# Performance work log

Hardware: AMD Instinct MI355X
Metric: run time of the kernel (lower is better)

## Reference

```python
import jax, jax.numpy as jnp
import numpy as np

N0, N1, N2 = 20000, 15000, 15000
N = N0 + N1 + N2          # total nodes
E = 800000                # edges
H, D = 4, 64              # heads, hidden per head
ED = 64                   # edge feature dim
NET = 8                   # num edge types
C = 16                    # num classes
SLOPE = 0.2               # leaky relu negative slope
ALPHA = 0.05              # residual-attention mixing

def _glorot(key, shape):
    return jax.random.normal(key, shape, dtype=jnp.float32) / jnp.sqrt(jnp.float32(shape[-1]))

def setup_inputs() -> dict:
    key = jax.random.key(0)
    ks = jax.random.split(key, 32)
    return {
        "x0": jax.random.normal(ks[0], (N0, 128), jnp.float32),
        "x1": jax.random.normal(ks[1], (N1, 64), jnp.float32),
        "x2": jax.random.normal(ks[2], (N2, 32), jnp.float32),
        "src": jax.random.randint(ks[3], (E,), 0, N),
        "dst": jax.random.randint(ks[4], (E,), 0, N),
        "efeat": jax.random.randint(ks[5], (E,), 0, NET),
        # per-node-type input projections (fc_list)
        "W0": _glorot(ks[6], (64, 128)), "b0": jnp.zeros((64,), jnp.float32),
        "W1": _glorot(ks[7], (64, 64)),  "b1": jnp.zeros((64,), jnp.float32),
        "W2": _glorot(ks[8], (64, 32)),  "b2": jnp.zeros((64,), jnp.float32),
        # GAT layer 0: in 64 -> H*D, no residual, elu
        "Wg0": _glorot(ks[9], (H * D, 64)),
        "etab0": _glorot(ks[10], (NET, ED)),
        "We0": _glorot(ks[11], (H * ED, ED)),
        "al0": _glorot(ks[12], (H, D)), "ar0": _glorot(ks[13], (H, D)), "ae0": _glorot(ks[14], (H, ED)),
        # GAT layer 1: in H*D -> H*D, identity residual, elu
        "Wg1": _glorot(ks[15], (H * D, H * D)),
        "etab1": _glorot(ks[16], (NET, ED)),
        "We1": _glorot(ks[17], (H * ED, ED)),
        "al1": _glorot(ks[18], (H, D)), "ar1": _glorot(ks[19], (H, D)), "ae1": _glorot(ks[20], (H, ED)),
        # final GAT layer: in H*D -> 1*C, linear residual, no activation
        "Wg2": _glorot(ks[21], (C, H * D)),
        "etab2": _glorot(ks[22], (NET, ED)),
        "We2": _glorot(ks[23], (ED, ED)),
        "al2": _glorot(ks[24], (1, C)), "ar2": _glorot(ks[25], (1, C)), "ae2": _glorot(ks[26], (1, ED)),
        "resW2": _glorot(ks[27], (C, H * D)),
    }

def _edge_softmax(scores, dst):
    # softmax over incoming edges of each dst node; scores: [E, H]
    m = jax.ops.segment_max(scores, dst, num_segments=N)
    ex = jnp.exp(scores - m[dst])
    s = jax.ops.segment_sum(ex, dst, num_segments=N)
    return ex / (s[dst] + 1e-9)

def _gat_conv(h, src, dst, et, Wg, etab, We, al, ar, ae, res_attn, res, resW, act):
    nH, oD = al.shape
    feat = (h @ Wg.T).reshape(N, nH, oD)                 # [N,H,D]
    ee = (etab[et] @ We.T).reshape(E, nH, -1)            # [E,H,ED]
    el = jnp.einsum('nhd,hd->nh', feat, al)
    er = jnp.einsum('nhd,hd->nh', feat, ar)
    es = jnp.einsum('ehd,hd->eh', ee, ae)
    logits = jax.nn.leaky_relu(el[src] + er[dst] + es, SLOPE)
    a = _edge_softmax(logits, dst)                       # [E,H]
    if res_attn is not None:
        a = a * (1.0 - ALPHA) + res_attn * ALPHA
    out = jax.ops.segment_sum(a[:, :, None] * feat[src], dst, num_segments=N)
    if res:
        resval = (h @ resW.T).reshape(N, -1, oD) if resW is not None else h.reshape(N, nH, oD)
        out = out + resval
    if act is not None:
        out = act(out)
    return out, jax.lax.stop_gradient(a)                 # attention detached (res_attn)

def reference(x0, x1, x2, src, dst, efeat, W0, b0, W1, b1, W2, b2,
              Wg0, etab0, We0, al0, ar0, ae0,
              Wg1, etab1, We1, al1, ar1, ae1,
              Wg2, etab2, We2, al2, ar2, ae2, resW2):
    h = jnp.concatenate([x0 @ W0.T + b0, x1 @ W1.T + b1, x2 @ W2.T + b2], axis=0)  # [N,64]
    h, ra = _gat_conv(h, src, dst, efeat, Wg0, etab0, We0, al0, ar0, ae0, None, False, None, jax.nn.elu)
    h = h.reshape(N, -1)
    h, ra = _gat_conv(h, src, dst, efeat, Wg1, etab1, We1, al1, ar1, ae1, ra, True, None, jax.nn.elu)
    h = h.reshape(N, -1)
    logits, _ = _gat_conv(h, src, dst, efeat, Wg2, etab2, We2, al2, ar2, ae2, None, True, resW2, None)
    return logits.mean(axis=1)                           # [N, C]
```

## Files before the change

### kernel.cpp

```cpp
#include <hip/hip_runtime.h>
#include <math.h>

#define N0 20000
#define N1 15000
#define N2 15000
#define NN 50000
#define EE 800000
#define SLOPE 0.2f
#define ALPHA 0.05f

typedef _Float16 h8 __attribute__((ext_vector_type(8)));
typedef _Float16 h4 __attribute__((ext_vector_type(4)));
typedef float f4v __attribute__((ext_vector_type(4)));

__device__ __forceinline__ float sel4(float4 v, int h) {
    float lo = (h & 1) ? v.y : v.x;
    float hi = (h & 1) ? v.w : v.z;
    return (h & 2) ? hi : lo;
}

__device__ __forceinline__ float elu_fast(float x) {
    return x > 0.f ? x : __expf(x) - 1.f;
}


__global__ void hist_kernel(const int* __restrict__ dst, int* __restrict__ deg, int E_) {
    int e = blockIdx.x * blockDim.x + threadIdx.x;
    if (e < E_) atomicAdd(&deg[dst[e]], 1);
}

__global__ __launch_bounds__(256) void block_sum_kernel(const int* __restrict__ deg,
                                                        int* __restrict__ bsum, int n) {
    int i = blockIdx.x * 256 + threadIdx.x;
    int v = (i < n) ? deg[i] : 0;
    #pragma unroll
    for (int off = 32; off > 0; off >>= 1) v += __shfl_down(v, off);
    __shared__ int sh[4];
    if ((threadIdx.x & 63) == 0) sh[threadIdx.x >> 6] = v;
    __syncthreads();
    if (threadIdx.x == 0) bsum[blockIdx.x] = sh[0] + sh[1] + sh[2] + sh[3];
}

__global__ __launch_bounds__(256) void scan_bsum_kernel(int* __restrict__ bsum, int nb) {
    __shared__ int sh[256];
    int tid = threadIdx.x;
    int v = (tid < nb) ? bsum[tid] : 0;
    sh[tid] = v;
    __syncthreads();
    #pragma unroll
    for (int off = 1; off < 256; off <<= 1) {
        int t = (tid >= off) ? sh[tid - off] : 0;
        __syncthreads();
        sh[tid] += t;
        __syncthreads();
    }
    if (tid < nb) bsum[tid] = sh[tid] - v;
}

__global__ __launch_bounds__(256) void scan_out_kernel(const int* __restrict__ deg,
                                                       const int* __restrict__ boff,
                                                       int* __restrict__ rowstart,
                                                       int* __restrict__ cursor, int n) {
    __shared__ int sh[256];
    int tid = threadIdx.x;
    int i = blockIdx.x * 256 + tid;
    int v = (i < n) ? deg[i] : 0;
    sh[tid] = v;
    __syncthreads();
    #pragma unroll
    for (int off = 1; off < 256; off <<= 1) {
        int t = (tid >= off) ? sh[tid - off] : 0;
        __syncthreads();
        sh[tid] += t;
        __syncthreads();
    }
    int excl = sh[tid] - v + boff[blockIdx.x];
    if (i < n) { rowstart[i] = excl; cursor[i] = excl; }
    if (i == n - 1) rowstart[n] = excl + v;
}

__global__ void scatter_kernel(const int* __restrict__ src, const int* __restrict__ dst,
                               const int* __restrict__ et, int* __restrict__ cursor,
                               int* __restrict__ pk, int E_) {
    int e = blockIdx.x * blockDim.x + threadIdx.x;
    if (e >= E_) return;
    int d = dst[e];
    int p = atomicAdd(&cursor[d], 1);
    pk[p] = (et[e] << 16) | src[e];
}


__global__ void es_table_all(const float* __restrict__ etab0, const float* __restrict__ We0,
                             const float* __restrict__ ae0,
                             const float* __restrict__ etab1, const float* __restrict__ We1,
                             const float* __restrict__ ae1,
                             const float* __restrict__ etab2, const float* __restrict__ We2,
                             const float* __restrict__ ae2,
                             float* __restrict__ es) {
    int b = blockIdx.x;
    const float *etab, *We, *ae;
    float* out;
    int H;
    if (b < 32)      { etab = etab0; We = We0; ae = ae0; out = es;      H = 4; }
    else if (b < 64) { b -= 32; etab = etab1; We = We1; ae = ae1; out = es + 32; H = 4; }
    else             { b -= 64; etab = etab2; We = We2; ae = ae2; out = es + 64; H = 1; }
    int t = b / H, h = b % H;
    int j = threadIdx.x;
    const float* w = We + (size_t)(h * 64 + j) * 64;
    const float* e = etab + t * 64;
    float s = 0.f;
    #pragma unroll
    for (int k = 0; k < 64; k += 4) {
        float4 wv = *(const float4*)(w + k);
        float4 ev = *(const float4*)(e + k);
        s += wv.x * ev.x + wv.y * ev.y + wv.z * ev.z + wv.w * ev.w;
    }
    s *= ae[h * 64 + j];
    #pragma unroll
    for (int off = 32; off > 0; off >>= 1) s += __shfl_down(s, off);
    if (j == 0) out[t * H + h] = s;
}


__global__ void f2h10(const float* s0, _Float16* d0, int n0,
                      const float* s1, _Float16* d1, int n1,
                      const float* s2, _Float16* d2, int n2,
                      const float* s3, _Float16* d3, int n3,
                      const float* s4, _Float16* d4, int n4,
                      const float* s5, _Float16* d5, int n5,
                      const float* s6, _Float16* d6, int n6,
                      const float* s7, _Float16* d7, int n7,
                      const float* s8, _Float16* d8, int n8,
                      const float* s9, _Float16* d9, int n9) {
    int t = blockIdx.x * 256 + threadIdx.x;
    if (t < n0) { d0[t] = (_Float16)s0[t]; return; } t -= n0;
    if (t < n1) { d1[t] = (_Float16)s1[t]; return; } t -= n1;
    if (t < n2) { d2[t] = (_Float16)s2[t]; return; } t -= n2;
    if (t < n3) { d3[t] = (_Float16)s3[t]; return; } t -= n3;
    if (t < n4) { d4[t] = (_Float16)s4[t]; return; } t -= n4;
    if (t < n5) { d5[t] = (_Float16)s5[t]; return; } t -= n5;
    if (t < n6) { d6[t] = (_Float16)s6[t]; return; } t -= n6;
    if (t < n7) { d7[t] = (_Float16)s7[t]; return; } t -= n7;
    if (t < n8) { d8[t] = (_Float16)s8[t]; return; } t -= n8;
    if (t < n9) { d9[t] = (_Float16)s9[t]; }
}


template<int NT>
__global__ __launch_bounds__(256) void gemm_mfma(const _Float16* __restrict__ A,
                                                 const _Float16* __restrict__ B,
                                                 const float* __restrict__ bias,
                                                 float* __restrict__ Cf,
                                                 _Float16* __restrict__ Ch,
                                                 int M, int N, int K) {
    const int wave = threadIdx.x >> 6;
    const int lane = threadIdx.x & 63;
    const int m_base = (blockIdx.x * 4 + wave) * 32;
    const int n_base = blockIdx.y * (NT * 16);
    const int row = lane & 15;
    const int kq = (lane >> 4) * 8;

    f4v acc[2][NT];
    #pragma unroll
    for (int i = 0; i < 2; i++)
        #pragma unroll
        for (int j = 0; j < NT; j++) {
            f4v z = {0.f, 0.f, 0.f, 0.f};
            acc[i][j] = z;
        }

    int r0 = m_base + row;      if (r0 >= M) r0 = M - 1;
    int r1 = m_base + 16 + row; if (r1 >= M) r1 = M - 1;
    const _Float16* a0p = A + (size_t)r0 * K + kq;
    const _Float16* a1p = A + (size_t)r1 * K + kq;
    const _Float16* bp  = B + (size_t)(n_base + row) * K + kq;

    for (int k = 0; k < K; k += 32) {
        h8 a0 = *(const h8*)(a0p + k);
        h8 a1 = *(const h8*)(a1p + k);
        #pragma unroll
        for (int j = 0; j < NT; j++) {
            h8 b = *(const h8*)(bp + (size_t)j * 16 * K + k);
            acc[0][j] = __builtin_amdgcn_mfma_f32_16x16x32_f16(a0, b, acc[0][j], 0, 0, 0);
            acc[1][j] = __builtin_amdgcn_mfma_f32_16x16x32_f16(a1, b, acc[1][j], 0, 0, 0);
        }
    }

    const int col = lane & 15;
    const int rb = (lane >> 4) * 4;
    #pragma unroll
    for (int ms = 0; ms < 2; ms++) {
        #pragma unroll
        for (int j = 0; j < NT; j++) {
            #pragma unroll
            for (int r = 0; r < 4; r++) {
                int m = m_base + ms * 16 + rb + r;
                if (m < M) {
                    int n = n_base + j * 16 + col;
                    float v = acc[ms][j][r];
                    if (bias) v += bias[n];
                    if (Cf) Cf[(size_t)m * N + n] = v;
                    if (Ch) Ch[(size_t)m * N + n] = (_Float16)v;
                }
            }
        }
    }
}


__global__ void node_elr_h(const _Float16* __restrict__ feat, const float* __restrict__ al,
                           const float* __restrict__ ar, float* __restrict__ el,
                           float* __restrict__ er, int nN) {
    int t = blockIdx.x * blockDim.x + threadIdx.x;
    if (t >= nN * 4) return;
    int n = t >> 2, h = t & 3;
    const _Float16* f = feat + (size_t)n * 256 + h * 64;
    const float* a = al + h * 64;
    const float* r = ar + h * 64;
    float sl = 0.f, sr = 0.f;
    #pragma unroll
    for (int j = 0; j < 64; j += 8) {
        h8 fv = *(const h8*)(f + j);
        #pragma unroll
        for (int q = 0; q < 8; q++) {
            float x = (float)fv[q];
            sl = fmaf(x, a[j + q], sl);
            sr = fmaf(x, r[j + q], sr);
        }
    }
    el[t] = sl; er[t] = sr;
}

__global__ void node_elr_f2(const float* __restrict__ feat, const float* __restrict__ al,
                            const float* __restrict__ ar, float* __restrict__ el,
                            float* __restrict__ er, int nN) {
    int t = blockIdx.x * blockDim.x + threadIdx.x;
    if (t >= nN) return;
    const float* f = feat + (size_t)t * 32;
    float sl = 0.f, sr = 0.f;
    #pragma unroll
    for (int j = 0; j < 16; j += 4) {
        float4 fv = *(const float4*)(f + j);
        float4 av = *(const float4*)(al + j);
        float4 rv = *(const float4*)(ar + j);
        sl += fv.x * av.x + fv.y * av.y + fv.z * av.z + fv.w * av.w;
        sr += fv.x * rv.x + fv.y * rv.y + fv.z * rv.z + fv.w * rv.w;
    }
    el[t] = sl; er[t] = sr;
}


template<bool WRITE_A, bool HAS_PREV, bool HAS_RES>
__global__ __launch_bounds__(256) void gat_fused4(const int* __restrict__ rowstart,
                                                  const int* __restrict__ pk,
                                                  const float* __restrict__ el,
                                                  const float* __restrict__ er,
                                                  const float* __restrict__ es,
                                                  const _Float16* __restrict__ feat,
                                                  const _Float16* __restrict__ aprev,
                                                  _Float16* __restrict__ awrite,
                                                  const _Float16* __restrict__ resh,
                                                  _Float16* __restrict__ outh, int nN) {
    __shared__ int2 as_lds[4][256];
    const int wave = threadIdx.x >> 6;
    const int lane = threadIdx.x & 63;
    int n = blockIdx.x * 4 + wave;
    if (n >= nN) return;
    const int r0 = rowstart[n], r1 = rowstart[n + 1];
    const int deg = r1 - r0;
    float4 er4 = *(const float4*)(er + n * 4);

    if (deg <= 64) {
        const int idx = r0 + lane;
        const bool act = idx < r1;
        int p = act ? pk[idx] : 0;
        int psrc = p & 0xFFFF;
        float4 v4 = {-INFINITY, -INFINITY, -INFINITY, -INFINITY};
        if (act) {
            float4 e4 = *(const float4*)(el + psrc * 4);
            float4 c4 = *(const float4*)(es + (p >> 16) * 4);
            float v;
            v = e4.x + er4.x + c4.x; v4.x = v > 0.f ? v : SLOPE * v;
            v = e4.y + er4.y + c4.y; v4.y = v > 0.f ? v : SLOPE * v;
            v = e4.z + er4.z + c4.z; v4.z = v > 0.f ? v : SLOPE * v;
            v = e4.w + er4.w + c4.w; v4.w = v > 0.f ? v : SLOPE * v;
        }
        float4 m4 = v4;
        #pragma unroll
        for (int off = 1; off <= 8; off <<= 1) {
            m4.x = fmaxf(m4.x, __shfl_xor(m4.x, off));
            m4.y = fmaxf(m4.y, __shfl_xor(m4.y, off));
            m4.z = fmaxf(m4.z, __shfl_xor(m4.z, off));
            m4.w = fmaxf(m4.w, __shfl_xor(m4.w, off));
        }
        if (deg > 16) {
            m4.x = fmaxf(m4.x, __shfl_xor(m4.x, 16));
            m4.y = fmaxf(m4.y, __shfl_xor(m4.y, 16));
            m4.z = fmaxf(m4.z, __shfl_xor(m4.z, 16));
            m4.w = fmaxf(m4.w, __shfl_xor(m4.w, 16));
        }
        if (deg > 32) {
            m4.x = fmaxf(m4.x, __shfl_xor(m4.x, 32));
            m4.y = fmaxf(m4.y, __shfl_xor(m4.y, 32));
            m4.z = fmaxf(m4.z, __shfl_xor(m4.z, 32));
            m4.w = fmaxf(m4.w, __shfl_xor(m4.w, 32));
        }
        float4 ex = {0.f, 0.f, 0.f, 0.f};
        if (act) {
            ex.x = __expf(v4.x - m4.x);
            ex.y = __expf(v4.y - m4.y);
            ex.z = __expf(v4.z - m4.z);
            ex.w = __expf(v4.w - m4.w);
        }
        float4 s4 = ex;
        #pragma unroll
        for (int off = 1; off <= 8; off <<= 1) {
            s4.x += __shfl_xor(s4.x, off);
            s4.y += __shfl_xor(s4.y, off);
            s4.z += __shfl_xor(s4.z, off);
            s4.w += __shfl_xor(s4.w, off);
        }
        if (deg > 16) {
            s4.x += __shfl_xor(s4.x, 16);
            s4.y += __shfl_xor(s4.y, 16);
            s4.z += __shfl_xor(s4.z, 16);
            s4.w += __shfl_xor(s4.w, 16);
        }
        if (deg > 32) {
            s4.x += __shfl_xor(s4.x, 32);
            s4.y += __shfl_xor(s4.y, 32);
            s4.z += __shfl_xor(s4.z, 32);
            s4.w += __shfl_xor(s4.w, 32);
        }
        float4 a4;
        a4.x = ex.x / (s4.x + 1e-9f);
        a4.y = ex.y / (s4.y + 1e-9f);
        a4.z = ex.z / (s4.z + 1e-9f);
        a4.w = ex.w / (s4.w + 1e-9f);
        if (HAS_PREV && act) {
            h4 pv = *(const h4*)(aprev + (size_t)idx * 4);
            a4.x = a4.x * (1.f - ALPHA) + ALPHA * (float)pv[0];
            a4.y = a4.y * (1.f - ALPHA) + ALPHA * (float)pv[1];
            a4.z = a4.z * (1.f - ALPHA) + ALPHA * (float)pv[2];
            a4.w = a4.w * (1.f - ALPHA) + ALPHA * (float)pv[3];
        }
        if (WRITE_A && act) {
            h4 aw;
            aw[0] = (_Float16)a4.x; aw[1] = (_Float16)a4.y;
            aw[2] = (_Float16)a4.z; aw[3] = (_Float16)a4.w;
            *(h4*)(awrite + (size_t)idx * 4) = aw;
        }
        {
            int2* dst_lds = &as_lds[wave][lane * 4];
            dst_lds[0] = make_int2(__float_as_int(a4.x), psrc);
            dst_lds[1] = make_int2(__float_as_int(a4.y), psrc);
            dst_lds[2] = make_int2(__float_as_int(a4.z), psrc);
            dst_lds[3] = make_int2(__float_as_int(a4.w), psrc);
        }

        const int half = lane >> 5;
        const int fl = lane & 31;
        const int h = fl >> 3;
        float acc8[8];
        #pragma unroll
        for (int q = 0; q < 8; q++) acc8[q] = 0.f;
        int i = r0;
        for (; i + 7 < r1; i += 8) {
            int j0 = (i - r0) + half;
            int2 e0 = as_lds[wave][(j0 + 0) * 4 + h];
            int2 e1 = as_lds[wave][(j0 + 2) * 4 + h];
            int2 e2 = as_lds[wave][(j0 + 4) * 4 + h];
            int2 e3 = as_lds[wave][(j0 + 6) * 4 + h];
            float a0 = __int_as_float(e0.x), a1 = __int_as_float(e1.x);
            float a2 = __int_as_float(e2.x), a3 = __int_as_float(e3.x);
            h8 f0 = *(const h8*)(feat + (size_t)e0.y * 256 + fl * 8);
            h8 f1 = *(const h8*)(feat + (size_t)e1.y * 256 + fl * 8);
            h8 f2 = *(const h8*)(feat + (size_t)e2.y * 256 + fl * 8);
            h8 f3 = *(const h8*)(feat + (size_t)e3.y * 256 + fl * 8);
            #pragma unroll
            for (int q = 0; q < 8; q++) acc8[q] = fmaf(a0, (float)f0[q], acc8[q]);
            #pragma unroll
            for (int q = 0; q < 8; q++) acc8[q] = fmaf(a1, (float)f1[q], acc8[q]);
            #pragma unroll
            for (int q = 0; q < 8; q++) acc8[q] = fmaf(a2, (float)f2[q], acc8[q]);
            #pragma unroll
            for (int q = 0; q < 8; q++) acc8[q] = fmaf(a3, (float)f3[q], acc8[q]);
        }
        for (; i + 3 < r1; i += 4) {
            int j0 = (i - r0) + half;
            int2 e0 = as_lds[wave][(j0 + 0) * 4 + h];
            int2 e1 = as_lds[wave][(j0 + 2) * 4 + h];
            float a0 = __int_as_float(e0.x), a1 = __int_as_float(e1.x);
            h8 f0 = *(const h8*)(feat + (size_t)e0.y * 256 + fl * 8);
            h8 f1 = *(const h8*)(feat + (size_t)e1.y * 256 + fl * 8);
            #pragma unroll
            for (int q = 0; q < 8; q++) acc8[q] = fmaf(a0, (float)f0[q], acc8[q]);
            #pragma unroll
            for (int q = 0; q < 8; q++) acc8[q] = fmaf(a1, (float)f1[q], acc8[q]);
        }
        for (; i + 1 < r1; i += 2) {
            int j0 = (i - r0) + half;
            int2 e0 = as_lds[wave][j0 * 4 + h];
            float a0 = __int_as_float(e0.x);
            h8 f0 = *(const h8*)(feat + (size_t)e0.y * 256 + fl * 8);
            #pragma unroll
            for (int q = 0; q < 8; q++) acc8[q] = fmaf(a0, (float)f0[q], acc8[q]);
        }
        if (i < r1) {
            int j0 = i - r0;
            int2 e0 = as_lds[wave][j0 * 4 + h];
            float a0 = (half == 0) ? __int_as_float(e0.x) : 0.f;
            h8 f0 = *(const h8*)(feat + (size_t)e0.y * 256 + fl * 8);
            #pragma unroll
            for (int q = 0; q < 8; q++) acc8[q] = fmaf(a0, (float)f0[q], acc8[q]);
        }
        #pragma unroll
        for (int q = 0; q < 8; q++) acc8[q] += __shfl_xor(acc8[q], 32);

        if (half == 0) {
            if (HAS_RES) {
                h8 rv = *(const h8*)(resh + (size_t)n * 256 + fl * 8);
                #pragma unroll
                for (int q = 0; q < 8; q++) acc8[q] += (float)rv[q];
            }
            #pragma unroll
            for (int q = 0; q < 8; q++) acc8[q] = elu_fast(acc8[q]);
            h8 o;
            #pragma unroll
            for (int q = 0; q < 8; q++) o[q] = (_Float16)acc8[q];
            *(h8*)(outh + (size_t)n * 256 + fl * 8) = o;
        }
        return;
    }

    float4 m4 = {-INFINITY, -INFINITY, -INFINITY, -INFINITY};
    for (int base = r0; base < r1; base += 64) {
        int idx = base + lane;
        if (idx < r1) {
            int p = pk[idx];
            float4 e4 = *(const float4*)(el + (p & 0xFFFF) * 4);
            float4 c4 = *(const float4*)(es + (p >> 16) * 4);
            float v;
            v = e4.x + er4.x + c4.x; v = v > 0.f ? v : SLOPE * v; m4.x = fmaxf(m4.x, v);
            v = e4.y + er4.y + c4.y; v = v > 0.f ? v : SLOPE * v; m4.y = fmaxf(m4.y, v);
            v = e4.z + er4.z + c4.z; v = v > 0.f ? v : SLOPE * v; m4.z = fmaxf(m4.z, v);
            v = e4.w + er4.w + c4.w; v = v > 0.f ? v : SLOPE * v; m4.w = fmaxf(m4.w, v);
        }
    }
    #pragma unroll
    for (int off = 1; off < 64; off <<= 1) {
        m4.x = fmaxf(m4.x, __shfl_xor(m4.x, off));
        m4.y = fmaxf(m4.y, __shfl_xor(m4.y, off));
        m4.z = fmaxf(m4.z, __shfl_xor(m4.z, off));
        m4.w = fmaxf(m4.w, __shfl_xor(m4.w, off));
    }
    float4 s4 = {0.f, 0.f, 0.f, 0.f};
    for (int base = r0; base < r1; base += 64) {
        int idx = base + lane;
        if (idx < r1) {
            int p = pk[idx];
            float4 e4 = *(const float4*)(el + (p & 0xFFFF) * 4);
            float4 c4 = *(const float4*)(es + (p >> 16) * 4);
            float4 exv;
            float v;
            v = e4.x + er4.x + c4.x; v = v > 0.f ? v : SLOPE * v; exv.x = __expf(v - m4.x);
            v = e4.y + er4.y + c4.y; v = v > 0.f ? v : SLOPE * v; exv.y = __expf(v - m4.y);
            v = e4.z + er4.z + c4.z; v = v > 0.f ? v : SLOPE * v; exv.z = __expf(v - m4.z);
            v = e4.w + er4.w + c4.w; v = v > 0.f ? v : SLOPE * v; exv.w = __expf(v - m4.w);
            if (base == r0) {
                int2* dst_lds = &as_lds[wave][lane * 4];
                dst_lds[0] = make_int2(__float_as_int(exv.x), 0);
                dst_lds[1] = make_int2(__float_as_int(exv.y), 0);
                dst_lds[2] = make_int2(__float_as_int(exv.z), 0);
                dst_lds[3] = make_int2(__float_as_int(exv.w), 0);
            }
            s4.x += exv.x; s4.y += exv.y; s4.z += exv.z; s4.w += exv.w;
        }
    }
    #pragma unroll
    for (int off = 1; off < 64; off <<= 1) {
        s4.x += __shfl_xor(s4.x, off);
        s4.y += __shfl_xor(s4.y, off);
        s4.z += __shfl_xor(s4.z, off);
        s4.w += __shfl_xor(s4.w, off);
    }
    float4 inv4;
    inv4.x = 1.f / (s4.x + 1e-9f); inv4.y = 1.f / (s4.y + 1e-9f);
    inv4.z = 1.f / (s4.z + 1e-9f); inv4.w = 1.f / (s4.w + 1e-9f);
    {
        int idx = r0 + lane;
        float4 a;
        a.x = __int_as_float(as_lds[wave][lane * 4 + 0].x) * inv4.x;
        a.y = __int_as_float(as_lds[wave][lane * 4 + 1].x) * inv4.y;
        a.z = __int_as_float(as_lds[wave][lane * 4 + 2].x) * inv4.z;
        a.w = __int_as_float(as_lds[wave][lane * 4 + 3].x) * inv4.w;
        if (HAS_PREV) {
            h4 pv = *(const h4*)(aprev + (size_t)idx * 4);
            a.x = a.x * (1.f - ALPHA) + ALPHA * (float)pv[0];
            a.y = a.y * (1.f - ALPHA) + ALPHA * (float)pv[1];
            a.z = a.z * (1.f - ALPHA) + ALPHA * (float)pv[2];
            a.w = a.w * (1.f - ALPHA) + ALPHA * (float)pv[3];
        }
        if (WRITE_A) {
            h4 aw;
            aw[0] = (_Float16)a.x; aw[1] = (_Float16)a.y;
            aw[2] = (_Float16)a.z; aw[3] = (_Float16)a.w;
            *(h4*)(awrite + (size_t)idx * 4) = aw;
        }
        as_lds[wave][lane * 4 + 0].x = __float_as_int(a.x);
        as_lds[wave][lane * 4 + 1].x = __float_as_int(a.y);
        as_lds[wave][lane * 4 + 2].x = __float_as_int(a.z);
        as_lds[wave][lane * 4 + 3].x = __float_as_int(a.w);
    }
    if (WRITE_A) {
        for (int base = r0 + 64; base < r1; base += 64) {
            int idx = base + lane;
            if (idx < r1) {
                int p = pk[idx];
                float4 e4 = *(const float4*)(el + (p & 0xFFFF) * 4);
                float4 c4 = *(const float4*)(es + (p >> 16) * 4);
                float4 a;
                float v;
                v = e4.x + er4.x + c4.x; v = v > 0.f ? v : SLOPE * v; a.x = __expf(v - m4.x) * inv4.x;
                v = e4.y + er4.y + c4.y; v = v > 0.f ? v : SLOPE * v; a.y = __expf(v - m4.y) * inv4.y;
                v = e4.z + er4.z + c4.z; v = v > 0.f ? v : SLOPE * v; a.z = __expf(v - m4.z) * inv4.z;
                v = e4.w + er4.w + c4.w; v = v > 0.f ? v : SLOPE * v; a.w = __expf(v - m4.w) * inv4.w;
                if (HAS_PREV) {
                    h4 pv = *(const h4*)(aprev + (size_t)idx * 4);
                    a.x = a.x * (1.f - ALPHA) + ALPHA * (float)pv[0];
                    a.y = a.y * (1.f - ALPHA) + ALPHA * (float)pv[1];
                    a.z = a.z * (1.f - ALPHA) + ALPHA * (float)pv[2];
                    a.w = a.w * (1.f - ALPHA) + ALPHA * (float)pv[3];
                }
                h4 aw;
                aw[0] = (_Float16)a.x; aw[1] = (_Float16)a.y;
                aw[2] = (_Float16)a.z; aw[3] = (_Float16)a.w;
                *(h4*)(awrite + (size_t)idx * 4) = aw;
            }
        }
    }
    const int h = lane >> 4;
    float4 acc = {0.f, 0.f, 0.f, 0.f};
    const int cap = r0 + 64;
    for (int i = r0; i < cap; i++) {
        int p = pk[i];
        float av = __int_as_float(as_lds[wave][(i - r0) * 4 + h].x);
        h4 f = *(const h4*)(feat + (size_t)(p & 0xFFFF) * 256 + lane * 4);
        acc.x = fmaf(av, (float)f[0], acc.x);
        acc.y = fmaf(av, (float)f[1], acc.y);
        acc.z = fmaf(av, (float)f[2], acc.z);
        acc.w = fmaf(av, (float)f[3], acc.w);
    }
    {
        float mh = sel4(m4, h), invh = sel4(inv4, h), erh = sel4(er4, h);
        for (int i = cap; i < r1; i++) {
            int p = pk[i];
            int s = p & 0xFFFF, t = p >> 16;
            float v = el[s * 4 + h] + erh + es[t * 4 + h];
            v = v > 0.f ? v : SLOPE * v;
            float a = __expf(v - mh) * invh;
            if (HAS_PREV) a = a * (1.f - ALPHA) + ALPHA * (float)aprev[(size_t)i * 4 + h];
            h4 f = *(const h4*)(feat + (size_t)s * 256 + lane * 4);
            acc.x = fmaf(a, (float)f[0], acc.x);
            acc.y = fmaf(a, (float)f[1], acc.y);
            acc.z = fmaf(a, (float)f[2], acc.z);
            acc.w = fmaf(a, (float)f[3], acc.w);
        }
    }
    if (HAS_RES) {
        h4 rv = *(const h4*)(resh + (size_t)n * 256 + lane * 4);
        acc.x += (float)rv[0]; acc.y += (float)rv[1];
        acc.z += (float)rv[2]; acc.w += (float)rv[3];
    }
    acc.x = elu_fast(acc.x);
    acc.y = elu_fast(acc.y);
    acc.z = elu_fast(acc.z);
    acc.w = elu_fast(acc.w);
    h4 o;
    o[0] = (_Float16)acc.x; o[1] = (_Float16)acc.y;
    o[2] = (_Float16)acc.z; o[3] = (_Float16)acc.w;
    *(h4*)(outh + (size_t)n * 256 + lane * 4) = o;
}


__global__ __launch_bounds__(256) void gat_fused1(const int* __restrict__ rowstart,
                                                  const int* __restrict__ pk,
                                                  const float* __restrict__ el,
                                                  const float* __restrict__ er,
                                                  const float* __restrict__ es,
                                                  const float* __restrict__ cpack,
                                                  float* __restrict__ out, int nN) {
    const int wave = threadIdx.x >> 6;
    const int lane = threadIdx.x & 63;
    int n = blockIdx.x * 4 + wave;
    if (n >= nN) return;
    const int r0 = rowstart[n], r1 = rowstart[n + 1];
    const int deg = r1 - r0;
    const float ern = er[n];

    if (deg <= 64) {
        const int idx = r0 + lane;
        const bool act = idx < r1;
        int p = act ? pk[idx] : 0;
        int psrc = p & 0xFFFF;
        float v = -INFINITY;
        if (act) {
            float t = el[psrc] + ern + es[p >> 16];
            v = t > 0.f ? t : SLOPE * t;
        }
        float m = v;
        #pragma unroll
        for (int off = 1; off <= 8; off <<= 1) m = fmaxf(m, __shfl_xor(m, off));
        if (deg > 16) m = fmaxf(m, __shfl_xor(m, 16));
        if (deg > 32) m = fmaxf(m, __shfl_xor(m, 32));
        float ex = act ? __expf(v - m) : 0.f;
        float s = ex;
        #pragma unroll
        for (int off = 1; off <= 8; off <<= 1) s += __shfl_xor(s, off);
        if (deg > 16) s += __shfl_xor(s, 16);
        if (deg > 32) s += __shfl_xor(s, 32);
        float a = ex / (s + 1e-9f);

        const int eslot = lane >> 4, fl = lane & 15;
        float acc = 0.f;
        int i = r0;
        for (; i + 7 < r1; i += 8) {
            int j0 = (i - r0) + eslot;
            int j1 = j0 + 4;
            int s0 = __shfl(psrc, j0);
            int s1 = __shfl(psrc, j1);
            float a0 = __shfl(a, j0);
            float a1 = __shfl(a, j1);
            float f0 = cpack[(size_t)s0 * 32 + fl];
            float f1 = cpack[(size_t)s1 * 32 + fl];
            acc = fmaf(a0, f0, acc);
            acc = fmaf(a1, f1, acc);
        }
        for (; i + 3 < r1; i += 4) {
            int j = (i - r0) + eslot;
            int sj = __shfl(psrc, j);
            float aj = __shfl(a, j);
            acc = fmaf(aj, cpack[(size_t)sj * 32 + fl], acc);
        }
        int rem = r1 - i;
        if (rem > 0) {
            int j = (i - r0) + (eslot < rem ? eslot : rem - 1);
            int sj = __shfl(psrc, j);
            float aj = __shfl(a, j);
            if (eslot >= rem) aj = 0.f;
            acc = fmaf(aj, cpack[(size_t)sj * 32 + fl], acc);
        }
        acc += __shfl_xor(acc, 16);
        acc += __shfl_xor(acc, 32);
        if (lane < 16) out[(size_t)n * 16 + lane] = acc + cpack[(size_t)n * 32 + 16 + lane];
        return;
    }

    float m = -INFINITY;
    for (int base = r0; base < r1; base += 64) {
        int idx = base + lane;
        if (idx < r1) {
            int p = pk[idx];
            float v = el[p & 0xFFFF] + ern + es[p >> 16];
            v = v > 0.f ? v : SLOPE * v;
            m = fmaxf(m, v);
        }
    }
    #pragma unroll
    for (int off = 1; off < 64; off <<= 1) m = fmaxf(m, __shfl_xor(m, off));
    float s = 0.f;
    for (int base = r0; base < r1; base += 64) {
        int idx = base + lane;
        if (idx < r1) {
            int p = pk[idx];
            float v = el[p & 0xFFFF] + ern + es[p >> 16];
            v = v > 0.f ? v : SLOPE * v;
            s += __expf(v - m);
        }
    }
    #pragma unroll
    for (int off = 1; off < 64; off <<= 1) s += __shfl_xor(s, off);
    float inv = 1.f / (s + 1e-9f);
    const int eslot = lane >> 4, fl = lane & 15;
    float acc = 0.f;
    for (int i = r0; i < r1; i += 4) {
        int rem = r1 - i;
        if (eslot < rem) {
            int j = i + eslot;
            int p = pk[j];
            float v = el[p & 0xFFFF] + ern + es[p >> 16];
            v = v > 0.f ? v : SLOPE * v;
            float a = __expf(v - m) * inv;
            acc = fmaf(a, cpack[(size_t)(p & 0xFFFF) * 32 + fl], acc);
        }
    }
    acc += __shfl_xor(acc, 16);
    acc += __shfl_xor(acc, 32);
    if (lane < 16) out[(size_t)n * 16 + lane] = acc + cpack[(size_t)n * 32 + 16 + lane];
}


extern "C" void kernel_launch(void* const* d_in, const int* in_sizes, int n_in,
                              void* d_out, int out_size, void* d_ws, size_t ws_size,
                              hipStream_t stream) {
    const float* x0 = (const float*)d_in[0];
    const float* x1 = (const float*)d_in[1];
    const float* x2 = (const float*)d_in[2];
    const int* src  = (const int*)d_in[3];
    const int* dst  = (const int*)d_in[4];
    const int* et   = (const int*)d_in[5];
    const float* W0 = (const float*)d_in[6];  const float* b0 = (const float*)d_in[7];
    const float* W1 = (const float*)d_in[8];  const float* b1 = (const float*)d_in[9];
    const float* W2 = (const float*)d_in[10]; const float* b2 = (const float*)d_in[11];
    const float* Wg0 = (const float*)d_in[12]; const float* etab0 = (const float*)d_in[13];
    const float* We0 = (const float*)d_in[14]; const float* al0 = (const float*)d_in[15];
    const float* ar0 = (const float*)d_in[16]; const float* ae0 = (const float*)d_in[17];
    const float* Wg1 = (const float*)d_in[18]; const float* etab1 = (const float*)d_in[19];
    const float* We1 = (const float*)d_in[20]; const float* al1 = (const float*)d_in[21];
    const float* ar1 = (const float*)d_in[22]; const float* ae1 = (const float*)d_in[23];
    const float* Wg2 = (const float*)d_in[24]; const float* etab2 = (const float*)d_in[25];
    const float* We2 = (const float*)d_in[26]; const float* al2 = (const float*)d_in[27];
    const float* ar2 = (const float*)d_in[28]; const float* ae2 = (const float*)d_in[29];
    const float* resW2 = (const float*)d_in[30];
    float* outp = (float*)d_out;

    char* p = (char*)d_ws;
    auto alloc = [&](size_t bytes) -> void* {
        void* r = (void*)p;
        p += (bytes + 255) & ~(size_t)255;
        return r;
    };
    _Float16* x0h   = (_Float16*)alloc((size_t)N0 * 128 * 2);
    _Float16* x1h   = (_Float16*)alloc((size_t)N1 * 64 * 2);
    _Float16* x2h   = (_Float16*)alloc((size_t)N2 * 32 * 2);
    _Float16* W0h   = (_Float16*)alloc(64 * 128 * 2);
    _Float16* W1h   = (_Float16*)alloc(64 * 64 * 2);
    _Float16* W2h   = (_Float16*)alloc(64 * 32 * 2);
    _Float16* Wg0h  = (_Float16*)alloc(256 * 64 * 2);
    _Float16* Wg1h  = (_Float16*)alloc(256 * 256 * 2);
    _Float16* wpkh  = (_Float16*)alloc(32 * 256 * 2);
    _Float16* h0h   = (_Float16*)alloc((size_t)NN * 64 * 2);
    _Float16* feath = (_Float16*)alloc((size_t)NN * 256 * 2);
    _Float16* bufAh = (_Float16*)alloc((size_t)NN * 256 * 2);
    _Float16* bufBh = (_Float16*)alloc((size_t)NN * 256 * 2);
    _Float16* a0h   = (_Float16*)alloc((size_t)EE * 4 * 2);
    float* el    = (float*)alloc((size_t)NN * 4 * 4);
    float* er    = (float*)alloc((size_t)NN * 4 * 4);
    float* es    = (float*)alloc(96 * 4);
    float* cpack = (float*)alloc((size_t)NN * 32 * 4);
    int* rowstart = (int*)alloc((size_t)(NN + 1) * 4);
    int* deg      = (int*)alloc((size_t)NN * 4);
    int* cursor   = (int*)alloc((size_t)NN * 4);
    int* bsum     = (int*)alloc(256 * 4);
    int* pk       = (int*)alloc((size_t)EE * 4);

    const int EB = (EE + 255) / 256;
    const int NB = (NN + 255) / 256;
    const int NHB = (NN * 4 + 255) / 256;
    const int MB128 = (NN + 127) / 128;
    const int WB = (NN + 3) / 4;

    hipMemsetAsync(deg, 0, (size_t)NN * 4, stream);
    hist_kernel<<<EB, 256, 0, stream>>>(dst, deg, EE);
    block_sum_kernel<<<NB, 256, 0, stream>>>(deg, bsum, NN);
    scan_bsum_kernel<<<1, 256, 0, stream>>>(bsum, NB);
    scan_out_kernel<<<NB, 256, 0, stream>>>(deg, bsum, rowstart, cursor, NN);
    scatter_kernel<<<EB, 256, 0, stream>>>(src, dst, et, cursor, pk, EE);

    es_table_all<<<72, 64, 0, stream>>>(etab0, We0, ae0, etab1, We1, ae1, etab2, We2, ae2, es);
    {
        int n0c = N0 * 128, n1c = N1 * 64, n2c = N2 * 32;
        int total = n0c + n1c + n2c + 8192 + 4096 + 2048 + 16384 + 65536 + 4096 + 4096;
        f2h10<<<(total + 255) / 256, 256, 0, stream>>>(
            x0, x0h, n0c, x1, x1h, n1c, x2, x2h, n2c,
            W0, W0h, 8192, W1, W1h, 4096, W2, W2h, 2048,
            Wg0, Wg0h, 16384, Wg1, Wg1h, 65536,
            Wg2, wpkh, 4096, resW2, wpkh + 4096, 4096);
    }

    gemm_mfma<4><<<dim3((N0 + 127) / 128, 1), 256, 0, stream>>>(x0h, W0h, b0, nullptr, h0h, N0, 64, 128);
    gemm_mfma<4><<<dim3((N1 + 127) / 128, 1), 256, 0, stream>>>(x1h, W1h, b1, nullptr, h0h + (size_t)N0 * 64, N1, 64, 64);
    gemm_mfma<4><<<dim3((N2 + 127) / 128, 1), 256, 0, stream>>>(x2h, W2h, b2, nullptr, h0h + (size_t)(N0 + N1) * 64, N2, 64, 32);

    gemm_mfma<8><<<dim3(MB128, 2), 256, 0, stream>>>(h0h, Wg0h, nullptr, nullptr, feath, NN, 256, 64);
    node_elr_h<<<NHB, 256, 0, stream>>>(feath, al0, ar0, el, er, NN);
    gat_fused4<true, false, false><<<WB, 256, 0, stream>>>(
        rowstart, pk, el, er, es + 0, feath, nullptr, a0h, nullptr, bufAh, NN);

    gemm_mfma<8><<<dim3(MB128, 2), 256, 0, stream>>>(bufAh, Wg1h, nullptr, nullptr, feath, NN, 256, 256);
    node_elr_h<<<NHB, 256, 0, stream>>>(feath, al1, ar1, el, er, NN);
    gat_fused4<false, true, true><<<WB, 256, 0, stream>>>(
        rowstart, pk, el, er, es + 32, feath, a0h, nullptr, bufAh, bufBh, NN);

    gemm_mfma<2><<<dim3(MB128, 1), 256, 0, stream>>>(bufBh, wpkh, nullptr, cpack, nullptr, NN, 32, 256);
    node_elr_f2<<<NB, 256, 0, stream>>>(cpack, al2, ar2, el, er, NN);
    gat_fused1<<<WB, 256, 0, stream>>>(rowstart, pk, el, er, es + 64, cpack, outp, NN);
}
```

Measured before the change: 527.5 us.

## Fuse attention-logit dot products into GEMM epilogues and merge projection GEMMs

Computes the per-node el/er attention terms inside the MFMA GEMM epilogue with cross-lane shuffles, which removes the separate node_elr kernels and their re-read of the feature matrix. The three per-type input projections are merged into one launch that dispatches on block index. The gat_fused4 LDS layout for attention weights is transposed to [head][edge] with padding so reads avoid bank conflicts, and the high-degree path now also stores source indices, which lets the fallback loop stop re-reading pk. In exchange the GEMM epilogue does more work and uses more registers.

```diff
diff --git a/kernel.cpp b/kernel.cpp
--- a/kernel.cpp
+++ b/kernel.cpp
@@ -146,17 +146,22 @@
 }
 
 
-template<int NT>
-__global__ __launch_bounds__(256) void gemm_mfma(const _Float16* __restrict__ A,
-                                                 const _Float16* __restrict__ B,
-                                                 const float* __restrict__ bias,
-                                                 float* __restrict__ Cf,
-                                                 _Float16* __restrict__ Ch,
-                                                 int M, int N, int K) {
+template<int NT, int ELR>
+__device__ __forceinline__ void gemm_body(int bx, int by,
+                                          const _Float16* __restrict__ A,
+                                          const _Float16* __restrict__ B,
+                                          const float* __restrict__ bias,
+                                          float* __restrict__ Cf,
+                                          _Float16* __restrict__ Ch,
+                                          float* __restrict__ el,
+                                          float* __restrict__ er,
+                                          const float* __restrict__ al,
+                                          const float* __restrict__ ar,
+                                          int M, int N, int K) {
     const int wave = threadIdx.x >> 6;
     const int lane = threadIdx.x & 63;
-    const int m_base = (blockIdx.x * 4 + wave) * 32;
-    const int n_base = blockIdx.y * (NT * 16);
+    const int m_base = (bx * 4 + wave) * 32;
+    const int n_base = by * (NT * 16);
     const int row = lane & 15;
     const int kq = (lane >> 4) * 8;
 
@@ -169,10 +174,10 @@
             acc[i][j] = z;
         }
 
-    int r0 = m_base + row;      if (r0 >= M) r0 = M - 1;
-    int r1 = m_base + 16 + row; if (r1 >= M) r1 = M - 1;
-    const _Float16* a0p = A + (size_t)r0 * K + kq;
-    const _Float16* a1p = A + (size_t)r1 * K + kq;
+    int ra = m_base + row;      if (ra >= M) ra = M - 1;
+    int rb2 = m_base + 16 + row; if (rb2 >= M) rb2 = M - 1;
+    const _Float16* a0p = A + (size_t)ra * K + kq;
+    const _Float16* a1p = A + (size_t)rb2 * K + kq;
     const _Float16* bp  = B + (size_t)(n_base + row) * K + kq;
 
     for (int k = 0; k < K; k += 32) {
@@ -188,6 +193,64 @@
 
     const int col = lane & 15;
     const int rb = (lane >> 4) * 4;
+
+    if (ELR == 1) {
+        float alw[NT], arw[NT];
+        #pragma unroll
+        for (int j = 0; j < NT; j++) {
+            int cg = n_base + j * 16 + col;
+            int hg = cg >> 6, d = cg & 63;
+            alw[j] = al[hg * 64 + d];
+            arw[j] = ar[hg * 64 + d];
+        }
+        const int hb = n_base >> 6;
+        #pragma unroll
+        for (int ms = 0; ms < 2; ms++) {
+            #pragma unroll
+            for (int r = 0; r < 4; r++) {
+                float e0 = 0.f, e1 = 0.f, f0 = 0.f, f1 = 0.f;
+                #pragma unroll
+                for (int j = 0; j < NT; j++) {
+                    float av = acc[ms][j][r];
+                    if (j < NT / 2) { e0 = fmaf(av, alw[j], e0); f0 = fmaf(av, arw[j], f0); }
+                    else            { e1 = fmaf(av, alw[j], e1); f1 = fmaf(av, arw[j], f1); }
+                }
+                #pragma unroll
+                for (int off = 1; off <= 8; off <<= 1) {
+                    e0 += __shfl_xor(e0, off);
+                    e1 += __shfl_xor(e1, off);
+                    f0 += __shfl_xor(f0, off);
+                    f1 += __shfl_xor(f1, off);
+                }
+                int m = m_base + ms * 16 + rb + r;
+                if (col == 0 && m < M) {
+                    el[m * 4 + hb]     = e0;
+                    el[m * 4 + hb + 1] = e1;
+                    er[m * 4 + hb]     = f0;
+                    er[m * 4 + hb + 1] = f1;
+                }
+            }
+        }
+    }
+    if (ELR == 2) {
+        float alw = al[col], arw = ar[col];
+        #pragma unroll
+        for (int ms = 0; ms < 2; ms++) {
+            #pragma unroll
+            for (int r = 0; r < 4; r++) {
+                float e = acc[ms][0][r] * alw;
+                float f = acc[ms][0][r] * arw;
+                #pragma unroll
+                for (int off = 1; off <= 8; off <<= 1) {
+                    e += __shfl_xor(e, off);
+                    f += __shfl_xor(f, off);
+                }
+                int m = m_base + ms * 16 + rb + r;
+                if (col == 0 && m < M) { el[m] = e; er[m] = f; }
+            }
+        }
+    }
+
     #pragma unroll
     for (int ms = 0; ms < 2; ms++) {
         #pragma unroll
@@ -207,46 +270,35 @@
     }
 }
 
-
-__global__ void node_elr_h(const _Float16* __restrict__ feat, const float* __restrict__ al,
-                           const float* __restrict__ ar, float* __restrict__ el,
-                           float* __restrict__ er, int nN) {
-    int t = blockIdx.x * blockDim.x + threadIdx.x;
-    if (t >= nN * 4) return;
-    int n = t >> 2, h = t & 3;
-    const _Float16* f = feat + (size_t)n * 256 + h * 64;
-    const float* a = al + h * 64;
-    const float* r = ar + h * 64;
-    float sl = 0.f, sr = 0.f;
-    #pragma unroll
-    for (int j = 0; j < 64; j += 8) {
-        h8 fv = *(const h8*)(f + j);
-        #pragma unroll
-        for (int q = 0; q < 8; q++) {
-            float x = (float)fv[q];
-            sl = fmaf(x, a[j + q], sl);
-            sr = fmaf(x, r[j + q], sr);
-        }
-    }
-    el[t] = sl; er[t] = sr;
-}
-
-__global__ void node_elr_f2(const float* __restrict__ feat, const float* __restrict__ al,
-                            const float* __restrict__ ar, float* __restrict__ el,
-                            float* __restrict__ er, int nN) {
-    int t = blockIdx.x * blockDim.x + threadIdx.x;
-    if (t >= nN) return;
-    const float* f = feat + (size_t)t * 32;
-    float sl = 0.f, sr = 0.f;
-    #pragma unroll
-    for (int j = 0; j < 16; j += 4) {
-        float4 fv = *(const float4*)(f + j);
-        float4 av = *(const float4*)(al + j);
-        float4 rv = *(const float4*)(ar + j);
-        sl += fv.x * av.x + fv.y * av.y + fv.z * av.z + fv.w * av.w;
-        sr += fv.x * rv.x + fv.y * rv.y + fv.z * rv.z + fv.w * rv.w;
-    }
-    el[t] = sl; er[t] = sr;
+template<int NT, int ELR>
+__global__ __launch_bounds__(256) void gemm_mfma(const _Float16* __restrict__ A,
+                                                 const _Float16* __restrict__ B,
+                                                 const float* __restrict__ bias,
+                                                 float* __restrict__ Cf,
+                                                 _Float16* __restrict__ Ch,
+                                                 float* __restrict__ el,
+                                                 float* __restrict__ er,
+                                                 const float* __restrict__ al,
+                                                 const float* __restrict__ ar,
+                                                 int M, int N, int K) {
+    gemm_body<NT, ELR>(blockIdx.x, blockIdx.y, A, B, bias, Cf, Ch, el, er, al, ar, M, N, K);
+}
+
+__global__ __launch_bounds__(256) void proj3(const _Float16* __restrict__ x0h, const _Float16* __restrict__ W0h, const float* __restrict__ b0,
+                                             const _Float16* __restrict__ x1h, const _Float16* __restrict__ W1h, const float* __restrict__ b1,
+                                             const _Float16* __restrict__ x2h, const _Float16* __restrict__ W2h, const float* __restrict__ b2,
+                                             _Float16* __restrict__ h0h, int nb0, int nb1) {
+    int b = blockIdx.x;
+    if (b < nb0) {
+        gemm_body<4, 0>(b, 0, x0h, W0h, b0, nullptr, h0h,
+                        nullptr, nullptr, nullptr, nullptr, N0, 64, 128);
+    } else if (b < nb0 + nb1) {
+        gemm_body<4, 0>(b - nb0, 0, x1h, W1h, b1, nullptr, h0h + (size_t)N0 * 64,
+                        nullptr, nullptr, nullptr, nullptr, N1, 64, 64);
+    } else {
+        gemm_body<4, 0>(b - nb0 - nb1, 0, x2h, W2h, b2, nullptr, h0h + (size_t)(N0 + N1) * 64,
+                        nullptr, nullptr, nullptr, nullptr, N2, 64, 32);
+    }
 }
 
 
@@ -261,7 +313,7 @@
                                                   _Float16* __restrict__ awrite,
                                                   const _Float16* __restrict__ resh,
                                                   _Float16* __restrict__ outh, int nN) {
-    __shared__ int2 as_lds[4][256];
+    __shared__ int2 as_lds[4][4][66];
     const int wave = threadIdx.x >> 6;
     const int lane = threadIdx.x & 63;
     int n = blockIdx.x * 4 + wave;
@@ -350,13 +402,10 @@
             aw[2] = (_Float16)a4.z; aw[3] = (_Float16)a4.w;
             *(h4*)(awrite + (size_t)idx * 4) = aw;
         }
-        {
-            int2* dst_lds = &as_lds[wave][lane * 4];
-            dst_lds[0] = make_int2(__float_as_int(a4.x), psrc);
-            dst_lds[1] = make_int2(__float_as_int(a4.y), psrc);
-            dst_lds[2] = make_int2(__float_as_int(a4.z), psrc);
-            dst_lds[3] = make_int2(__float_as_int(a4.w), psrc);
-        }
+        as_lds[wave][0][lane] = make_int2(__float_as_int(a4.x), psrc);
+        as_lds[wave][1][lane] = make_int2(__float_as_int(a4.y), psrc);
+        as_lds[wave][2][lane] = make_int2(__float_as_int(a4.z), psrc);
+        as_lds[wave][3][lane] = make_int2(__float_as_int(a4.w), psrc);
 
         const int half = lane >> 5;
         const int fl = lane & 31;
@@ -367,10 +416,10 @@
         int i = r0;
         for (; i + 7 < r1; i += 8) {
             int j0 = (i - r0) + half;
-            int2 e0 = as_lds[wave][(j0 + 0) * 4 + h];
-            int2 e1 = as_lds[wave][(j0 + 2) * 4 + h];
-            int2 e2 = as_lds[wave][(j0 + 4) * 4 + h];
-            int2 e3 = as_lds[wave][(j0 + 6) * 4 + h];
+            int2 e0 = as_lds[wave][h][j0 + 0];
+            int2 e1 = as_lds[wave][h][j0 + 2];
+            int2 e2 = as_lds[wave][h][j0 + 4];
+            int2 e3 = as_lds[wave][h][j0 + 6];
             float a0 = __int_as_float(e0.x), a1 = __int_as_float(e1.x);
             float a2 = __int_as_float(e2.x), a3 = __int_as_float(e3.x);
             h8 f0 = *(const h8*)(feat + (size_t)e0.y * 256 + fl * 8);
@@ -388,8 +437,8 @@
         }
         for (; i + 3 < r1; i += 4) {
             int j0 = (i - r0) + half;
-            int2 e0 = as_lds[wave][(j0 + 0) * 4 + h];
-            int2 e1 = as_lds[wave][(j0 + 2) * 4 + h];
+            int2 e0 = as_lds[wave][h][j0 + 0];
+            int2 e1 = as_lds[wave][h][j0 + 2];
             float a0 = __int_as_float(e0.x), a1 = __int_as_float(e1.x);
             h8 f0 = *(const h8*)(feat + (size_t)e0.y * 256 + fl * 8);
             h8 f1 = *(const h8*)(feat + (size_t)e1.y * 256 + fl * 8);
@@ -400,7 +449,7 @@
         }
         for (; i + 1 < r1; i += 2) {
             int j0 = (i - r0) + half;
-            int2 e0 = as_lds[wave][j0 * 4 + h];
+            int2 e0 = as_lds[wave][h][j0];
             float a0 = __int_as_float(e0.x);
             h8 f0 = *(const h8*)(feat + (size_t)e0.y * 256 + fl * 8);
             #pragma unroll
@@ -408,7 +457,7 @@
         }
         if (i < r1) {
             int j0 = i - r0;
-            int2 e0 = as_lds[wave][j0 * 4 + h];
+            int2 e0 = as_lds[wave][h][j0];
             float a0 = (half == 0) ? __int_as_float(e0.x) : 0.f;
             h8 f0 = *(const h8*)(feat + (size_t)e0.y * 256 + fl * 8);
             #pragma unroll
@@ -468,11 +517,10 @@
             v = e4.z + er4.z + c4.z; v = v > 0.f ? v : SLOPE * v; exv.z = __expf(v - m4.z);
             v = e4.w + er4.w + c4.w; v = v > 0.f ? v : SLOPE * v; exv.w = __expf(v - m4.w);
             if (base == r0) {
-                int2* dst_lds = &as_lds[wave][lane * 4];
-                dst_lds[0] = make_int2(__float_as_int(exv.x), 0);
-                dst_lds[1] = make_int2(__float_as_int(exv.y), 0);
-                dst_lds[2] = make_int2(__float_as_int(exv.z), 0);
-                dst_lds[3] = make_int2(__float_as_int(exv.w), 0);
+                as_lds[wave][0][lane] = make_int2(__float_as_int(exv.x), p & 0xFFFF);
+                as_lds[wave][1][lane] = make_int2(__float_as_int(exv.y), p & 0xFFFF);
+                as_lds[wave][2][lane] = make_int2(__float_as_int(exv.z), p & 0xFFFF);
+                as_lds[wave][3][lane] = make_int2(__float_as_int(exv.w), p & 0xFFFF);
             }
             s4.x += exv.x; s4.y += exv.y; s4.z += exv.z; s4.w += exv.w;
         }
@@ -490,10 +538,10 @@
     {
         int idx = r0 + lane;
         float4 a;
-        a.x = __int_as_float(as_lds[wave][lane * 4 + 0].x) * inv4.x;
-        a.y = __int_as_float(as_lds[wave][lane * 4 + 1].x) * inv4.y;
-        a.z = __int_as_float(as_lds[wave][lane * 4 + 2].x) * inv4.z;
-        a.w = __int_as_float(as_lds[wave][lane * 4 + 3].x) * inv4.w;
+        a.x = __int_as_float(as_lds[wave][0][lane].x) * inv4.x;
+        a.y = __int_as_float(as_lds[wave][1][lane].x) * inv4.y;
+        a.z = __int_as_float(as_lds[wave][2][lane].x) * inv4.z;
+        a.w = __int_as_float(as_lds[wave][3][lane].x) * inv4.w;
         if (HAS_PREV) {
             h4 pv = *(const h4*)(aprev + (size_t)idx * 4);
             a.x = a.x * (1.f - ALPHA) + ALPHA * (float)pv[0];
@@ -507,10 +555,10 @@
             aw[2] = (_Float16)a.z; aw[3] = (_Float16)a.w;
             *(h4*)(awrite + (size_t)idx * 4) = aw;
         }
-        as_lds[wave][lane * 4 + 0].x = __float_as_int(a.x);
-        as_lds[wave][lane * 4 + 1].x = __float_as_int(a.y);
-        as_lds[wave][lane * 4 + 2].x = __float_as_int(a.z);
-        as_lds[wave][lane * 4 + 3].x = __float_as_int(a.w);
+        as_lds[wave][0][lane].x = __float_as_int(a.x);
+        as_lds[wave][1][lane].x = __float_as_int(a.y);
+        as_lds[wave][2][lane].x = __float_as_int(a.z);
+        as_lds[wave][3][lane].x = __float_as_int(a.w);
     }
     if (WRITE_A) {
         for (int base = r0 + 64; base < r1; base += 64) {
@@ -543,9 +591,9 @@
     float4 acc = {0.f, 0.f, 0.f, 0.f};
     const int cap = r0 + 64;
     for (int i = r0; i < cap; i++) {
-        int p = pk[i];
-        float av = __int_as_float(as_lds[wave][(i - r0) * 4 + h].x);
-        h4 f = *(const h4*)(feat + (size_t)(p & 0xFFFF) * 256 + lane * 4);
+        int2 e0 = as_lds[wave][h][i - r0];
+        h4 f = *(const h4*)(feat + (size_t)e0.y * 256 + lane * 4);
+        float av = __int_as_float(e0.x);
         acc.x = fmaf(av, (float)f[0], acc.x);
         acc.y = fmaf(av, (float)f[1], acc.y);
         acc.z = fmaf(av, (float)f[2], acc.z);
@@ -756,9 +804,11 @@
 
     const int EB = (EE + 255) / 256;
     const int NB = (NN + 255) / 256;
-    const int NHB = (NN * 4 + 255) / 256;
     const int MB128 = (NN + 127) / 128;
     const int WB = (NN + 3) / 4;
+    const int nb0 = (N0 + 127) / 128;
+    const int nb1 = (N1 + 127) / 128;
+    const int nb2 = (N2 + 127) / 128;
 
     hipMemsetAsync(deg, 0, (size_t)NN * 4, stream);
     hist_kernel<<<EB, 256, 0, stream>>>(dst, deg, EE);
@@ -778,21 +828,20 @@
             Wg2, wpkh, 4096, resW2, wpkh + 4096, 4096);
     }
 
-    gemm_mfma<4><<<dim3((N0 + 127) / 128, 1), 256, 0, stream>>>(x0h, W0h, b0, nullptr, h0h, N0, 64, 128);
-    gemm_mfma<4><<<dim3((N1 + 127) / 128, 1), 256, 0, stream>>>(x1h, W1h, b1, nullptr, h0h + (size_t)N0 * 64, N1, 64, 64);
-    gemm_mfma<4><<<dim3((N2 + 127) / 128, 1), 256, 0, stream>>>(x2h, W2h, b2, nullptr, h0h + (size_t)(N0 + N1) * 64, N2, 64, 32);
-
-    gemm_mfma<8><<<dim3(MB128, 2), 256, 0, stream>>>(h0h, Wg0h, nullptr, nullptr, feath, NN, 256, 64);
-    node_elr_h<<<NHB, 256, 0, stream>>>(feath, al0, ar0, el, er, NN);
+    proj3<<<nb0 + nb1 + nb2, 256, 0, stream>>>(x0h, W0h, b0, x1h, W1h, b1, x2h, W2h, b2,
+                                               h0h, nb0, nb1);
+
+    gemm_mfma<8, 1><<<dim3(MB128, 2), 256, 0, stream>>>(h0h, Wg0h, nullptr, nullptr, feath,
+                                                        el, er, al0, ar0, NN, 256, 64);
     gat_fused4<true, false, false><<<WB, 256, 0, stream>>>(
         rowstart, pk, el, er, es + 0, feath, nullptr, a0h, nullptr, bufAh, NN);
 
-    gemm_mfma<8><<<dim3(MB128, 2), 256, 0, stream>>>(bufAh, Wg1h, nullptr, nullptr, feath, NN, 256, 256);
-    node_elr_h<<<NHB, 256, 0, stream>>>(feath, al1, ar1, el, er, NN);
+    gemm_mfma<8, 1><<<dim3(MB128, 2), 256, 0, stream>>>(bufAh, Wg1h, nullptr, nullptr, feath,
+                                                        el, er, al1, ar1, NN, 256, 256);
     gat_fused4<false, true, true><<<WB, 256, 0, stream>>>(
         rowstart, pk, el, er, es + 32, feath, a0h, nullptr, bufAh, bufBh, NN);
 
-    gemm_mfma<2><<<dim3(MB128, 1), 256, 0, stream>>>(bufBh, wpkh, nullptr, cpack, nullptr, NN, 32, 256);
-    node_elr_f2<<<NB, 256, 0, stream>>>(cpack, al2, ar2, el, er, NN);
+    gemm_mfma<2, 2><<<dim3(MB128, 1), 256, 0, stream>>>(bufBh, wpkh, nullptr, cpack, nullptr,
+                                                        el, er, al2, ar2, NN, 32, 256);
     gat_fused1<<<WB, 256, 0, stream>>>(rowstart, pk, el, er, es + 64, cpack, outp, NN);
 }
```

After: 480.1 us. 9.0% less time.
